# Kernel tuning notes

Measured on AMD Instinct MI355X. Metric: run time of the kernel, lower is better.

The kernel has to match this reference:

```python
import jax, jax.numpy as jnp
import numpy as np

VOCAB, E, H1, H2, T = 32000, 256, 256, 256, 12
START, STOP = 10, 11
B, S = 32, 512


def _lstm_dir(x, Wih, Whh, bih, bhh):
    # x: [S, B, D]; PyTorch gate order i, f, g, o
    Bsz = x.shape[1]
    H = Whh.shape[1]
    def step(carry, xt):
        h, c = carry
        z = xt @ Wih.T + h @ Whh.T + bih + bhh  # [B, 4H]
        i, f, g, o = jnp.split(z, 4, axis=-1)
        c = jax.nn.sigmoid(f) * c + jax.nn.sigmoid(i) * jnp.tanh(g)
        h = jax.nn.sigmoid(o) * jnp.tanh(c)
        return (h, c), h
    h0 = jnp.zeros((Bsz, H), x.dtype)
    _, hs = jax.lax.scan(step, (h0, h0), x)
    return hs


def _bilstm(x, pf, pb):
    hf = _lstm_dir(x, *pf)
    hb = _lstm_dir(x[::-1], *pb)[::-1]
    return jnp.concatenate([hf, hb], axis=-1)


def _attention(x, attW):
    # faithful to source: x is time-major [S, B, 2H1]; Attention treats dim0 as batch
    w = x @ attW.T                                   # W(word_embs)
    scores = jnp.einsum('abd,acd->abc', w, x)        # [S, B, B]
    weights = jax.nn.softmax(scores, axis=-1)
    g = jnp.einsum('abc,acd->abd', weights, x)       # [S, B, 2H1]
    return jnp.concatenate([w, g], axis=-1)          # [S, B, 4H1]


def _features(inputs, emb, p1f, p1b, attW, p2f, p2b, h2t_W, h2t_b):
    x = emb[inputs]                       # [B, S, E] (row 0 zeroed = padding_idx)
    x = jnp.swapaxes(x, 0, 1)             # [S, B, E] time-major
    h1 = _bilstm(x, p1f, p1b)             # [S, B, 2*H1]
    a = _attention(h1, attW)              # [S, B, 4*H1]
    h2 = _bilstm(a, p2f, p2b)             # [S, B, 2*H2]
    feats = h2 @ h2t_W.T + h2t_b          # [S, B, T]
    return jnp.swapaxes(feats, 0, 1)      # [B, S, T]


def _viterbi(feats, transitions):
    # feats: [B, S, T]; transitions[next, prev]
    Bsz = feats.shape[0]
    init = jnp.full((Bsz, T), -10000.0, feats.dtype).at[:, START].set(0.0)
    def step(fv, feat_t):
        scores = fv[:, None, :] + transitions[None, :, :]  # [B, next, prev]
        bptr = jnp.argmax(scores, axis=-1)                 # [B, T]
        fv_new = jnp.max(scores, axis=-1) + feat_t
        return fv_new, bptr
    fv, bptrs = jax.lax.scan(step, init, jnp.swapaxes(feats, 0, 1))  # bptrs [S, B, T]
    terminal = fv + transitions[STOP][None, :]
    best_last = jnp.argmax(terminal, axis=-1)  # [B]
    def back(tag, bp_t):
        prev = jnp.take_along_axis(bp_t, tag[:, None], axis=1)[:, 0]
        return prev, tag
    _, path = jax.lax.scan(back, best_last, bptrs, reverse=True)  # [S, B]
    return jnp.swapaxes(path, 0, 1)  # [B, S]


def setup_inputs() -> dict:
    key = jax.random.key(0)
    ks = jax.random.split(key, 24)
    sc = 0.1
    d = {}
    d['inputs'] = jax.random.randint(ks[0], (B, S), 0, VOCAB, dtype=jnp.int32)
    emb = sc * jax.random.normal(ks[1], (VOCAB, E), jnp.float32)
    d['emb'] = emb.at[0].set(0.0)  # padding_idx=0
    # lstm_1 (input E, hidden H1), forward and backward directions
    d['w1f_ih'] = sc * jax.random.normal(ks[2], (4 * H1, E), jnp.float32)
    d['w1f_hh'] = sc * jax.random.normal(ks[3], (4 * H1, H1), jnp.float32)
    d['b1f_ih'] = sc * jax.random.normal(ks[4], (4 * H1,), jnp.float32)
    d['b1f_hh'] = sc * jax.random.normal(ks[5], (4 * H1,), jnp.float32)
    d['w1b_ih'] = sc * jax.random.normal(ks[6], (4 * H1, E), jnp.float32)
    d['w1b_hh'] = sc * jax.random.normal(ks[7], (4 * H1, H1), jnp.float32)
    d['b1b_ih'] = sc * jax.random.normal(ks[8], (4 * H1,), jnp.float32)
    d['b1b_hh'] = sc * jax.random.normal(ks[9], (4 * H1,), jnp.float32)
    d['attW'] = sc * jax.random.normal(ks[10], (2 * H1, 2 * H1), jnp.float32)
    # lstm_2 (input 4*H1, hidden H2)
    d['w2f_ih'] = sc * jax.random.normal(ks[11], (4 * H2, 4 * H1), jnp.float32)
    d['w2f_hh'] = sc * jax.random.normal(ks[12], (4 * H2, H2), jnp.float32)
    d['b2f_ih'] = sc * jax.random.normal(ks[13], (4 * H2,), jnp.float32)
    d['b2f_hh'] = sc * jax.random.normal(ks[14], (4 * H2,), jnp.float32)
    d['w2b_ih'] = sc * jax.random.normal(ks[15], (4 * H2, 4 * H1), jnp.float32)
    d['w2b_hh'] = sc * jax.random.normal(ks[16], (4 * H2, H2), jnp.float32)
    d['b2b_ih'] = sc * jax.random.normal(ks[17], (4 * H2,), jnp.float32)
    d['b2b_hh'] = sc * jax.random.normal(ks[18], (4 * H2,), jnp.float32)
    d['h2t_W'] = sc * jax.random.normal(ks[19], (T, 2 * H2), jnp.float32)
    d['h2t_b'] = sc * jax.random.normal(ks[20], (T,), jnp.float32)
    tr = jax.random.normal(ks[21], (T, T), jnp.float32)
    tr = tr.at[START, :].set(-10000.0).at[:, STOP].set(-10000.0)
    d['transitions'] = tr
    return d


def reference(inputs, emb, w1f_ih, w1f_hh, b1f_ih, b1f_hh, w1b_ih, w1b_hh, b1b_ih, b1b_hh,
              attW, w2f_ih, w2f_hh, b2f_ih, b2f_hh, w2b_ih, w2b_hh, b2b_ih, b2b_hh,
              h2t_W, h2t_b, transitions):
    feats = _features(inputs, emb,
                      (w1f_ih, w1f_hh, b1f_ih, b1f_hh), (w1b_ih, w1b_hh, b1b_ih, b1b_hh),
                      attW,
                      (w2f_ih, w2f_hh, b2f_ih, b2f_hh), (w2b_ih, w2b_hh, b2b_ih, b2b_hh),
                      h2t_W, h2t_b)
    return _viterbi(feats, transitions)  # [B, S] int tag sequences
```

## Files before the change

### kernel.cpp

```cpp
#include <hip/hip_runtime.h>

#define SEQ 512
#define BATCH 32
#define NTAG 12
#define STOP_TAG 11

static __device__ __forceinline__ float sigm(float x) {
  return 1.0f / (1.0f + __expf(-x));
}
static __device__ __forceinline__ float tanh_fast(float x) {
  return 1.0f - 2.0f / (1.0f + __expf(2.0f * x));
}

__global__ __launch_bounds__(64) void embed_kernel(const int* __restrict__ inputs,
                                                   const float* __restrict__ emb,
                                                   float* __restrict__ x0) {
  const int sb = blockIdx.x;
  const int s = sb >> 5, b = sb & 31;
  const int tok = inputs[b * SEQ + s];
  const float4* src = (const float4*)(emb + (size_t)tok * 256);
  float4* dst = (float4*)(x0 + (size_t)sb * 256);
  dst[threadIdx.x] = src[threadIdx.x];
}

__global__ __launch_bounds__(256) void gemm128(const float* __restrict__ A,
                                               const float* __restrict__ W,
                                               const float* __restrict__ b1,
                                               const float* __restrict__ b2,
                                               float* __restrict__ C,
                                               int M, int N, int K, int ldc) {
  __shared__ float aT[16][132];
  __shared__ float wT[16][140];
  const int tid = threadIdx.x;
  const int bm = blockIdx.x * 128;
  const int bn = blockIdx.y * 128;
  const int tm = (tid >> 4) << 3;
  const int tn = (tid & 15) << 3;
  const int pn = tn + ((tn >> 5) & 3) * 4;
  const int lr = tid >> 1;
  const int lk = (tid & 1) << 3;
  const int plr = lr + ((lr >> 5) & 3) * 4;
  const float* __restrict__ aSrc = A + (size_t)(bm + lr) * K + lk;
  const float* __restrict__ wSrc = W + (size_t)(bn + lr) * K + lk;
  float acc[8][8] = {{0.f}};
  for (int k0 = 0; k0 < K; k0 += 16) {
    const float4 av0 = *(const float4*)(aSrc + k0);
    const float4 av1 = *(const float4*)(aSrc + k0 + 4);
    const float4 wv0 = *(const float4*)(wSrc + k0);
    const float4 wv1 = *(const float4*)(wSrc + k0 + 4);
    __syncthreads();
    aT[lk + 0][lr] = av0.x; aT[lk + 1][lr] = av0.y; aT[lk + 2][lr] = av0.z; aT[lk + 3][lr] = av0.w;
    aT[lk + 4][lr] = av1.x; aT[lk + 5][lr] = av1.y; aT[lk + 6][lr] = av1.z; aT[lk + 7][lr] = av1.w;
    wT[lk + 0][plr] = wv0.x; wT[lk + 1][plr] = wv0.y; wT[lk + 2][plr] = wv0.z; wT[lk + 3][plr] = wv0.w;
    wT[lk + 4][plr] = wv1.x; wT[lk + 5][plr] = wv1.y; wT[lk + 6][plr] = wv1.z; wT[lk + 7][plr] = wv1.w;
    __syncthreads();
#pragma unroll
    for (int k = 0; k < 16; ++k) {
      const float4 a0 = *(const float4*)&aT[k][tm];
      const float4 a1 = *(const float4*)&aT[k][tm + 4];
      const float4 w0 = *(const float4*)&wT[k][pn];
      const float4 w1 = *(const float4*)&wT[k][pn + 4];
      const float a[8] = {a0.x, a0.y, a0.z, a0.w, a1.x, a1.y, a1.z, a1.w};
      const float w[8] = {w0.x, w0.y, w0.z, w0.w, w1.x, w1.y, w1.z, w1.w};
#pragma unroll
      for (int i = 0; i < 8; ++i)
#pragma unroll
        for (int j = 0; j < 8; ++j)
          acc[i][j] = fmaf(a[i], w[j], acc[i][j]);
    }
  }
  float bias[8];
#pragma unroll
  for (int j = 0; j < 8; ++j) {
    const int n = bn + tn + j;
    bias[j] = (b1 ? b1[n] : 0.f) + (b2 ? b2[n] : 0.f);
  }
#pragma unroll
  for (int i = 0; i < 8; ++i) {
    float* row = C + (size_t)(bm + tm + i) * ldc + bn + tn;
    *(float4*)(row) = make_float4(acc[i][0] + bias[0], acc[i][1] + bias[1],
                                  acc[i][2] + bias[2], acc[i][3] + bias[3]);
    *(float4*)(row + 4) = make_float4(acc[i][4] + bias[4], acc[i][5] + bias[5],
                                      acc[i][6] + bias[6], acc[i][7] + bias[7]);
  }
}

__global__ __launch_bounds__(256) void gemm_nt(const float* __restrict__ A,
                                               const float* __restrict__ W,
                                               const float* __restrict__ b1,
                                               const float* __restrict__ b2,
                                               float* __restrict__ C,
                                               int M, int N, int K, int ldc) {
  __shared__ float aT[16][68];
  __shared__ float wT[16][68];
  const int tid = threadIdx.x;
  const int bm = blockIdx.x * 64;
  const int bn = blockIdx.y * 64;
  const int tm = ((tid >> 4) & 15) << 2;
  const int tn = (tid & 15) << 2;
  const int lr = tid >> 2;
  const int lk = (tid & 3) << 2;
  const bool wok = (bn + lr) < N;
  float acc00 = 0.f, acc01 = 0.f, acc02 = 0.f, acc03 = 0.f;
  float acc10 = 0.f, acc11 = 0.f, acc12 = 0.f, acc13 = 0.f;
  float acc20 = 0.f, acc21 = 0.f, acc22 = 0.f, acc23 = 0.f;
  float acc30 = 0.f, acc31 = 0.f, acc32 = 0.f, acc33 = 0.f;
  for (int k0 = 0; k0 < K; k0 += 16) {
    float4 av = *(const float4*)(A + (size_t)(bm + lr) * K + k0 + lk);
    float4 wv = make_float4(0.f, 0.f, 0.f, 0.f);
    if (wok) wv = *(const float4*)(W + (size_t)(bn + lr) * K + k0 + lk);
    aT[lk + 0][lr] = av.x; aT[lk + 1][lr] = av.y; aT[lk + 2][lr] = av.z; aT[lk + 3][lr] = av.w;
    wT[lk + 0][lr] = wv.x; wT[lk + 1][lr] = wv.y; wT[lk + 2][lr] = wv.z; wT[lk + 3][lr] = wv.w;
    __syncthreads();
#pragma unroll
    for (int k = 0; k < 16; ++k) {
      float4 a4 = *(const float4*)&aT[k][tm];
      float4 w4 = *(const float4*)&wT[k][tn];
      acc00 += a4.x * w4.x; acc01 += a4.x * w4.y; acc02 += a4.x * w4.z; acc03 += a4.x * w4.w;
      acc10 += a4.y * w4.x; acc11 += a4.y * w4.y; acc12 += a4.y * w4.z; acc13 += a4.y * w4.w;
      acc20 += a4.z * w4.x; acc21 += a4.z * w4.y; acc22 += a4.z * w4.z; acc23 += a4.z * w4.w;
      acc30 += a4.w * w4.x; acc31 += a4.w * w4.y; acc32 += a4.w * w4.z; acc33 += a4.w * w4.w;
    }
    __syncthreads();
  }
  float r[4][4] = {{acc00, acc01, acc02, acc03},
                   {acc10, acc11, acc12, acc13},
                   {acc20, acc21, acc22, acc23},
                   {acc30, acc31, acc32, acc33}};
#pragma unroll
  for (int i = 0; i < 4; ++i) {
#pragma unroll
    for (int j = 0; j < 4; ++j) {
      int n = bn + tn + j;
      if (n < N) {
        float v = r[i][j];
        if (b1) v += b1[n];
        if (b2) v += b2[n];
        C[(size_t)(bm + tm + i) * ldc + n] = v;
      }
    }
  }
}

__global__ __launch_bounds__(256, 1) void lstm_scan(const float* __restrict__ pre_f,
                                                    const float* __restrict__ pre_b,
                                                    const float* __restrict__ whh_f,
                                                    const float* __restrict__ whh_b,
                                                    float* __restrict__ hs,
                                                    float* __restrict__ hx,
                                                    unsigned int* __restrict__ claim) {
  const int tid = threadIdx.x;
  __shared__ int s_lin;
  if (tid == 0) {
    const unsigned xcd = __builtin_amdgcn_s_getreg(6164) & 7u;
    int lin = 0;
    for (int i = 0; i < 256; ++i) {
      const int cand = (int)((xcd * 32 + i) & 255);
      unsigned exp = 0u;
      if (__hip_atomic_compare_exchange_strong(&claim[cand], &exp, 1u,
            __ATOMIC_RELAXED, __ATOMIC_RELAXED, __HIP_MEMORY_SCOPE_AGENT)) {
        lin = cand;
        break;
      }
    }
    s_lin = lin;
  }
  __syncthreads();
  const int lin = s_lin;
  const int pair = lin >> 2;
  const int q = lin & 3;
  const int dir = pair >> 5;
  const int b = pair & 31;
  const float* __restrict__ pre = dir ? pre_b : pre_f;
  const float* __restrict__ whh = dir ? whh_b : whh_f;
  const int u = tid & 63;
  const int col = (tid >> 6) * 256 + (q << 6) + u;
  float* hx_w = hx + pair * 512;

  __shared__ float4 stage[8192];
  __shared__ float hbuf[2][256];
  __shared__ float zbuf[256];

  for (int it = 0; it < 32; ++it) {
    const int id = (it << 8) + tid;
    const int lc = id >> 5;
    const int g = id & 31;
    const int gcol = ((lc >> 6) << 8) + (q << 6) + (lc & 63);
    stage[(lc << 5) | (g ^ (lc & 31))] = *((const float4*)(whh + (size_t)gcol * 256) + g);
  }
  __syncthreads();
  float4 wv[64];
#pragma unroll
  for (int g = 0; g < 32; ++g)
    wv[g] = stage[(tid << 5) | (g ^ (tid & 31))];
  __syncthreads();
  for (int it = 0; it < 32; ++it) {
    const int id = (it << 8) + tid;
    const int lc = id >> 5;
    const int g = id & 31;
    const int gcol = ((lc >> 6) << 8) + (q << 6) + (lc & 63);
    stage[(lc << 5) | (g ^ (lc & 31))] = *((const float4*)(whh + (size_t)gcol * 256) + 32 + g);
  }
  __syncthreads();
#pragma unroll
  for (int g = 0; g < 32; ++g)
    wv[32 + g] = stage[(tid << 5) | (g ^ (tid & 31))];

  hbuf[0][tid] = 0.0f;
  hbuf[1][tid] = 0.0f;
  float c_reg = 0.0f;
  const int sfirst = dir ? (SEQ - 1) : 0;
  float p = pre[((size_t)(sfirst * BATCH) + b) * 1024 + col];
  __syncthreads();

  for (int t = 0; t < SEQ; ++t) {
    const int s = dir ? (SEQ - 1 - t) : t;
    float np = 0.0f;
    if (t + 1 < SEQ) {
      const int sn = dir ? (s - 1) : (s + 1);
      np = pre[((size_t)(sn * BATCH) + b) * 1024 + col];
    }
    if (t > 0) {
      if (tid < 192) {
        const int pq = (q + 1 + (tid >> 6)) & 3;
        const int slot = (pq << 6) + (tid & 63);
        const float ef = 2.0f * (float)((t - 1) & 3);
        const float* addr = hx_w + ((t - 1) & 1) * 256 + slot;
        float v;
        int spin = 0;
        while (true) {
          if (spin < 16) {
            asm volatile("global_load_dword %0, %1, off sc0\n\t"
                         "s_waitcnt vmcnt(0)"
                         : "=v"(v) : "v"(addr));
          } else {
            v = __hip_atomic_load(addr, __ATOMIC_RELAXED, __HIP_MEMORY_SCOPE_AGENT);
          }
          if (__builtin_fabsf(v - ef) <= 1.0f) break;
          ++spin;
          if (spin > 4) __builtin_amdgcn_s_sleep(1);
        }
        hbuf[t & 1][slot] = v - ef;
      }
      __syncthreads();
    }
    float a0 = p, a1 = 0.f, a2 = 0.f, a3 = 0.f;
    const float4* hb = (const float4*)hbuf[t & 1];
#pragma unroll
    for (int g = 0; g < 64; ++g) {
      const float4 h4 = hb[g];
      a0 = fmaf(h4.x, wv[g].x, a0);
      a1 = fmaf(h4.y, wv[g].y, a1);
      a2 = fmaf(h4.z, wv[g].z, a2);
      a3 = fmaf(h4.w, wv[g].w, a3);
    }
    zbuf[tid] = (a0 + a1) + (a2 + a3);
    __syncthreads();
    if (tid < 64) {
      const float zi = zbuf[u];
      const float zf = zbuf[64 + u];
      const float zg = zbuf[128 + u];
      const float zo = zbuf[192 + u];
      c_reg = sigm(zf) * c_reg + sigm(zi) * tanh_fast(zg);
      const float h = sigm(zo) * tanh_fast(c_reg);
      __hip_atomic_store(hx_w + (t & 1) * 256 + (q << 6) + u, h + 2.0f * (float)(t & 3),
                         __ATOMIC_RELAXED, __HIP_MEMORY_SCOPE_AGENT);
      hbuf[(t + 1) & 1][(q << 6) + u] = h;
      hs[((size_t)(s * BATCH) + b) * 512 + dir * 256 + (q << 6) + u] = h;
    }
    p = np;
  }
}

__global__ __launch_bounds__(256) void attention_kernel(const float* __restrict__ h1s,
                                                        float* __restrict__ att) {
  const int s = blockIdx.x;
  __shared__ float wl[32][512];
  __shared__ float xT[512][36];
  __shared__ float sc[32][33];
  const int tid = threadIdx.x;
#pragma unroll
  for (int r = 0; r < 16; ++r) {
    int flat = r * 1024 + tid * 4;
    int bb = flat >> 9;
    int d = flat & 511;
    float4 wv = *(const float4*)(att + ((size_t)(s * BATCH) + bb) * 1024 + d);
    *(float4*)&wl[bb][d] = wv;
    float4 xv = *(const float4*)(h1s + ((size_t)(s * BATCH) + bb) * 512 + d);
    xT[d + 0][bb] = xv.x; xT[d + 1][bb] = xv.y; xT[d + 2][bb] = xv.z; xT[d + 3][bb] = xv.w;
  }
  __syncthreads();
  {
    const int i = tid >> 3;
    const int j0 = (tid & 7) << 2;
    float a0 = 0.f, a1 = 0.f, a2 = 0.f, a3 = 0.f;
    for (int k = 0; k < 512; ++k) {
      float wv = wl[i][k];
      float4 x4 = *(const float4*)&xT[k][j0];
      a0 += wv * x4.x; a1 += wv * x4.y; a2 += wv * x4.z; a3 += wv * x4.w;
    }
    sc[i][j0 + 0] = a0; sc[i][j0 + 1] = a1; sc[i][j0 + 2] = a2; sc[i][j0 + 3] = a3;
  }
  __syncthreads();
  if (tid < 32) {
    float m = -3.4e38f;
    for (int j = 0; j < 32; ++j) m = fmaxf(m, sc[tid][j]);
    float sum = 0.f;
    for (int j = 0; j < 32; ++j) { float ev = __expf(sc[tid][j] - m); sc[tid][j] = ev; sum += ev; }
    float inv = 1.0f / sum;
    for (int j = 0; j < 32; ++j) sc[tid][j] *= inv;
  }
  __syncthreads();
  {
    const int i = tid >> 3;
    const int dq = tid & 7;
#pragma unroll
    for (int rep = 0; rep < 8; ++rep) {
      const int d0 = dq * 64 + rep * 8;
      float g0 = 0.f, g1 = 0.f, g2 = 0.f, g3 = 0.f, g4 = 0.f, g5 = 0.f, g6 = 0.f, g7 = 0.f;
      for (int j = 0; j < 32; ++j) {
        float wt = sc[i][j];
        g0 += wt * xT[d0 + 0][j]; g1 += wt * xT[d0 + 1][j];
        g2 += wt * xT[d0 + 2][j]; g3 += wt * xT[d0 + 3][j];
        g4 += wt * xT[d0 + 4][j]; g5 += wt * xT[d0 + 5][j];
        g6 += wt * xT[d0 + 6][j]; g7 += wt * xT[d0 + 7][j];
      }
      float* o = att + ((size_t)(s * BATCH) + i) * 1024 + 512 + d0;
      *(float4*)(o) = make_float4(g0, g1, g2, g3);
      *(float4*)(o + 4) = make_float4(g4, g5, g6, g7);
    }
  }
}

__global__ __launch_bounds__(64) void viterbi_kernel(const float* __restrict__ feats,
                                                     const float* __restrict__ trans,
                                                     int* __restrict__ out) {
  const int b = blockIdx.x;
  __shared__ float tl[NTAG][NTAG];
  __shared__ float fv[2][NTAG];
  __shared__ unsigned char bp[SEQ][NTAG];
  const int tid = threadIdx.x;
  for (int i = tid; i < NTAG * NTAG; i += 64) tl[i / NTAG][i % NTAG] = trans[i];
  if (tid < NTAG) fv[0][tid] = (tid == 10) ? 0.f : -10000.f;
  __syncthreads();
  for (int t = 0; t < SEQ; ++t) {
    const int cur = t & 1;
    if (tid < NTAG) {
      float m = -3.4e38f;
      int arg = 0;
      for (int p = 0; p < NTAG; ++p) {
        float v = fv[cur][p] + tl[tid][p];
        if (v > m) { m = v; arg = p; }
      }
      bp[t][tid] = (unsigned char)arg;
      fv[cur ^ 1][tid] = m + feats[((size_t)t * BATCH + b) * NTAG + tid];
    }
    __syncthreads();
  }
  if (tid == 0) {
    float m = -3.4e38f;
    int tag = 0;
    for (int p = 0; p < NTAG; ++p) {
      float v = fv[0][p] + tl[STOP_TAG][p];
      if (v > m) { m = v; tag = p; }
    }
    for (int t = SEQ - 1; t >= 0; --t) {
      out[b * SEQ + t] = tag;
      tag = bp[t][tag];
    }
  }
}

extern "C" void kernel_launch(void* const* d_in, const int* in_sizes, int n_in,
                              void* d_out, int out_size, void* d_ws, size_t ws_size,
                              hipStream_t stream) {
  const int* inputs = (const int*)d_in[0];
  const float* emb = (const float*)d_in[1];
  const float* w1f_ih = (const float*)d_in[2];
  const float* w1f_hh = (const float*)d_in[3];
  const float* b1f_ih = (const float*)d_in[4];
  const float* b1f_hh = (const float*)d_in[5];
  const float* w1b_ih = (const float*)d_in[6];
  const float* w1b_hh = (const float*)d_in[7];
  const float* b1b_ih = (const float*)d_in[8];
  const float* b1b_hh = (const float*)d_in[9];
  const float* attW = (const float*)d_in[10];
  const float* w2f_ih = (const float*)d_in[11];
  const float* w2f_hh = (const float*)d_in[12];
  const float* b2f_ih = (const float*)d_in[13];
  const float* b2f_hh = (const float*)d_in[14];
  const float* w2b_ih = (const float*)d_in[15];
  const float* w2b_hh = (const float*)d_in[16];
  const float* b2b_ih = (const float*)d_in[17];
  const float* b2b_hh = (const float*)d_in[18];
  const float* h2t_W = (const float*)d_in[19];
  const float* h2t_b = (const float*)d_in[20];
  const float* trans = (const float*)d_in[21];

  float* ws = (float*)d_ws;
  float* preF = ws;
  float* preB = ws + 16777216;
  float* h1s  = ws + 33554432;
  float* att  = ws + 41943040;
  float* x0   = ws + 58720256;
  float* feats = x0;
  float* hx1  = ws + 62914560;
  float* hx2  = ws + 62947328;
  unsigned int* claim1 = (unsigned int*)(ws + 62980096);
  unsigned int* claim2 = (unsigned int*)(ws + 62980352);
  int* out = (int*)d_out;

  hipMemsetAsync(hx1, 0xFF, 2 * 32768 * sizeof(float), stream);
  hipMemsetAsync(claim1, 0, 2 * 256 * sizeof(unsigned int), stream);
  embed_kernel<<<SEQ * BATCH, 64, 0, stream>>>(inputs, emb, x0);
  gemm128<<<dim3(128, 8), 256, 0, stream>>>(x0, w1f_ih, b1f_ih, b1f_hh, preF, 16384, 1024, 256, 1024);
  gemm128<<<dim3(128, 8), 256, 0, stream>>>(x0, w1b_ih, b1b_ih, b1b_hh, preB, 16384, 1024, 256, 1024);
  lstm_scan<<<256, 256, 0, stream>>>(preF, preB, w1f_hh, w1b_hh, h1s, hx1, claim1);
  gemm128<<<dim3(128, 4), 256, 0, stream>>>(h1s, attW, nullptr, nullptr, att, 16384, 512, 512, 1024);
  attention_kernel<<<SEQ, 256, 0, stream>>>(h1s, att);
  gemm128<<<dim3(128, 8), 256, 0, stream>>>(att, w2f_ih, b2f_ih, b2f_hh, preF, 16384, 1024, 1024, 1024);
  gemm128<<<dim3(128, 8), 256, 0, stream>>>(att, w2b_ih, b2b_ih, b2b_hh, preB, 16384, 1024, 1024, 1024);
  lstm_scan<<<256, 256, 0, stream>>>(preF, preB, w2f_hh, w2b_hh, h1s, hx2, claim2);
  gemm_nt<<<dim3(256, 1), 256, 0, stream>>>(h1s, h2t_W, h2t_b, nullptr, feats, 16384, 12, 512, 12);
  viterbi_kernel<<<BATCH, 64, 0, stream>>>(feats, trans, out);
}
```

Baseline: 5.996 ms.

## Use split-bf16 MFMA GEMM for layer-2 LSTM input projections

Converts the attention output and layer-2 input weights into hi/lo bf16 pairs and computes the two large 16384x1024x1024 input projections with bf16 MFMA instructions, using three products per tile (hi*hi, hi*lo, lo*hi) to approximate fp32 accuracy. The aim is to replace the scalar fp32 tiled GEMM with matrix-core throughput. In exchange it adds conversion kernels and extra workspace traffic, reuses existing buffers as scratch, and keeps slightly lower precision than full fp32, which could flip argmax decisions in Viterbi.

```diff
diff --git a/kernel.cpp b/kernel.cpp
--- a/kernel.cpp
+++ b/kernel.cpp
@@ -5,11 +5,18 @@
 #define NTAG 12
 #define STOP_TAG 11
 
+typedef __attribute__((ext_vector_type(8))) short bs8;
+typedef __attribute__((ext_vector_type(4))) float fx4;
+
 static __device__ __forceinline__ float sigm(float x) {
   return 1.0f / (1.0f + __expf(-x));
 }
 static __device__ __forceinline__ float tanh_fast(float x) {
   return 1.0f - 2.0f / (1.0f + __expf(2.0f * x));
+}
+static __device__ __forceinline__ ushort bf16_rne(float x) {
+  unsigned u = __float_as_uint(x);
+  return (ushort)((u + 0x7FFFu + ((u >> 16) & 1u)) >> 16);
 }
 
 __global__ __launch_bounds__(64) void embed_kernel(const int* __restrict__ inputs,
@@ -21,6 +28,103 @@
   const float4* src = (const float4*)(emb + (size_t)tok * 256);
   float4* dst = (float4*)(x0 + (size_t)sb * 256);
   dst[threadIdx.x] = src[threadIdx.x];
+}
+
+__global__ __launch_bounds__(256) void cvt_hilo(const float* __restrict__ in,
+                                                ushort* __restrict__ hi,
+                                                ushort* __restrict__ lo, int n4) {
+  const int stride = gridDim.x * 256;
+  for (int i = blockIdx.x * 256 + threadIdx.x; i < n4; i += stride) {
+    float4 v = ((const float4*)in)[i];
+    float vv[4] = {v.x, v.y, v.z, v.w};
+    ushort h[4], l[4];
+#pragma unroll
+    for (int j = 0; j < 4; ++j) {
+      ushort hb = bf16_rne(vv[j]);
+      float hf = __uint_as_float(((unsigned)hb) << 16);
+      h[j] = hb;
+      l[j] = bf16_rne(vv[j] - hf);
+    }
+    ((ushort4*)hi)[i] = make_ushort4(h[0], h[1], h[2], h[3]);
+    ((ushort4*)lo)[i] = make_ushort4(l[0], l[1], l[2], l[3]);
+  }
+}
+
+__global__ __launch_bounds__(256) void gemm_mfma(const ushort* __restrict__ Ah,
+                                                 const ushort* __restrict__ Al,
+                                                 const ushort* __restrict__ Wh,
+                                                 const ushort* __restrict__ Wl,
+                                                 const float* __restrict__ b1,
+                                                 const float* __restrict__ b2,
+                                                 float* __restrict__ C,
+                                                 int M, int N, int K) {
+  __shared__ ushort lAh[128 * 40];
+  __shared__ ushort lAl[128 * 40];
+  __shared__ ushort lWh[128 * 40];
+  __shared__ ushort lWl[128 * 40];
+  const int tid = threadIdx.x;
+  const int bm = blockIdx.x * 128;
+  const int bn = blockIdx.y * 128;
+  const int w = tid >> 6, lane = tid & 63;
+  const int wr = (w >> 1) * 64, wc = (w & 1) * 64;
+  const int r16 = lane & 15, q = lane >> 4;
+  const int srow = tid & 127, shalf = tid >> 7;
+  const size_t aBase = (size_t)(bm + srow) * K + 16 * shalf;
+  const size_t wBase = (size_t)(bn + srow) * K + 16 * shalf;
+  const int ldst = srow * 40 + 16 * shalf;
+  fx4 acc[4][4];
+#pragma unroll
+  for (int i = 0; i < 4; ++i)
+#pragma unroll
+    for (int j = 0; j < 4; ++j) {
+      fx4 z = {0.f, 0.f, 0.f, 0.f};
+      acc[i][j] = z;
+    }
+  for (int k0 = 0; k0 < K; k0 += 32) {
+    const float4 ah0 = *(const float4*)(Ah + aBase + k0);
+    const float4 ah1 = *(const float4*)(Ah + aBase + k0 + 8);
+    const float4 al0 = *(const float4*)(Al + aBase + k0);
+    const float4 al1 = *(const float4*)(Al + aBase + k0 + 8);
+    const float4 wh0 = *(const float4*)(Wh + wBase + k0);
+    const float4 wh1 = *(const float4*)(Wh + wBase + k0 + 8);
+    const float4 wl0 = *(const float4*)(Wl + wBase + k0);
+    const float4 wl1 = *(const float4*)(Wl + wBase + k0 + 8);
+    __syncthreads();
+    *(float4*)&lAh[ldst] = ah0; *(float4*)&lAh[ldst + 8] = ah1;
+    *(float4*)&lAl[ldst] = al0; *(float4*)&lAl[ldst + 8] = al1;
+    *(float4*)&lWh[ldst] = wh0; *(float4*)&lWh[ldst + 8] = wh1;
+    *(float4*)&lWl[ldst] = wl0; *(float4*)&lWl[ldst + 8] = wl1;
+    __syncthreads();
+    bs8 fah[4], fal[4], fwh[4], fwl[4];
+#pragma unroll
+    for (int i = 0; i < 4; ++i) {
+      const int ao = (wr + 16 * i + r16) * 40 + 8 * q;
+      fah[i] = *(const bs8*)&lAh[ao];
+      fal[i] = *(const bs8*)&lAl[ao];
+      const int wo = (wc + 16 * i + r16) * 40 + 8 * q;
+      fwh[i] = *(const bs8*)&lWh[wo];
+      fwl[i] = *(const bs8*)&lWl[wo];
+    }
+#pragma unroll
+    for (int i = 0; i < 4; ++i)
+#pragma unroll
+      for (int j = 0; j < 4; ++j) {
+        acc[i][j] = __builtin_amdgcn_mfma_f32_16x16x32_bf16(fah[i], fwh[j], acc[i][j], 0, 0, 0);
+        acc[i][j] = __builtin_amdgcn_mfma_f32_16x16x32_bf16(fah[i], fwl[j], acc[i][j], 0, 0, 0);
+        acc[i][j] = __builtin_amdgcn_mfma_f32_16x16x32_bf16(fal[i], fwh[j], acc[i][j], 0, 0, 0);
+      }
+  }
+#pragma unroll
+  for (int i = 0; i < 4; ++i)
+#pragma unroll
+    for (int j = 0; j < 4; ++j) {
+      const int crow = bm + wr + 16 * i + 4 * q;
+      const int ccol = bn + wc + 16 * j + r16;
+      const float bias = b1[ccol] + b2[ccol];
+#pragma unroll
+      for (int r = 0; r < 4; ++r)
+        C[(size_t)(crow + r) * N + ccol] = acc[i][j][r] + bias;
+    }
 }
 
 __global__ __launch_bounds__(256) void gemm128(const float* __restrict__ A,
@@ -408,6 +512,13 @@
   float* hx2  = ws + 62947328;
   unsigned int* claim1 = (unsigned int*)(ws + 62980096);
   unsigned int* claim2 = (unsigned int*)(ws + 62980352);
+  ushort* atth = (ushort*)h1s;
+  ushort* attl = (ushort*)preB;
+  ushort* w2fh = (ushort*)x0;
+  ushort* w2fl = (ushort*)(x0 + 524288);
+  ushort* w2bh = (ushort*)(x0 + 1048576);
+  ushort* w2bl = (ushort*)(x0 + 1572864);
+  float* preB2 = att;
   int* out = (int*)d_out;
 
   hipMemsetAsync(hx1, 0xFF, 2 * 32768 * sizeof(float), stream);
@@ -418,9 +529,12 @@
   lstm_scan<<<256, 256, 0, stream>>>(preF, preB, w1f_hh, w1b_hh, h1s, hx1, claim1);
   gemm128<<<dim3(128, 4), 256, 0, stream>>>(h1s, attW, nullptr, nullptr, att, 16384, 512, 512, 1024);
   attention_kernel<<<SEQ, 256, 0, stream>>>(h1s, att);
-  gemm128<<<dim3(128, 8), 256, 0, stream>>>(att, w2f_ih, b2f_ih, b2f_hh, preF, 16384, 1024, 1024, 1024);
-  gemm128<<<dim3(128, 8), 256, 0, stream>>>(att, w2b_ih, b2b_ih, b2b_hh, preB, 16384, 1024, 1024, 1024);
-  lstm_scan<<<256, 256, 0, stream>>>(preF, preB, w2f_hh, w2b_hh, h1s, hx2, claim2);
+  cvt_hilo<<<4096, 256, 0, stream>>>(att, atth, attl, 4194304);
+  cvt_hilo<<<512, 256, 0, stream>>>(w2f_ih, w2fh, w2fl, 262144);
+  cvt_hilo<<<512, 256, 0, stream>>>(w2b_ih, w2bh, w2bl, 262144);
+  gemm_mfma<<<dim3(128, 8), 256, 0, stream>>>(atth, attl, w2fh, w2fl, b2f_ih, b2f_hh, preF, 16384, 1024, 1024);
+  gemm_mfma<<<dim3(128, 8), 256, 0, stream>>>(atth, attl, w2bh, w2bl, b2b_ih, b2b_hh, preB2, 16384, 1024, 1024);
+  lstm_scan<<<256, 256, 0, stream>>>(preF, preB2, w2f_hh, w2b_hh, h1s, hx2, claim2);
   gemm_nt<<<dim3(256, 1), 256, 0, stream>>>(h1s, h2t_W, h2t_b, nullptr, feats, 16384, 12, 512, 12);
   viterbi_kernel<<<BATCH, 64, 0, stream>>>(feats, trans, out);
 }
```

New measurement: 5.497 ms. 1.09x faster.
